# Kernel optimization log

Hardware: AMD Instinct MI355X
Metric: run time of the kernel (lower is better)

## Reference

```python
import jax, jax.numpy as jnp
import numpy as np

N_NODES = 50000
N_EDGES = 1_600_000
DIMS = [512, 2048, 1024, 512]  # input, hiddens..., output
NEG_SLOPE = 0.2
EPS = 1e-12


def setup_inputs() -> dict:
    key = jax.random.key(0)
    ks = jax.random.split(key, 12)
    inp = {
        "x": jax.random.normal(ks[0], (N_NODES, DIMS[0]), dtype=jnp.float32),
        "edge_row": jax.random.randint(ks[1], (N_EDGES,), 0, N_NODES, dtype=jnp.int32),
        "edge_col": jax.random.randint(ks[2], (N_EDGES,), 0, N_NODES, dtype=jnp.int32),
        "edge_val": jax.random.uniform(ks[3], (N_EDGES,), dtype=jnp.float32),
    }
    # GraphConvolution params per layer: W [d_in, d_out], b [d_out]
    for i in range(len(DIMS) - 1):
        d_in, d_out = DIMS[i], DIMS[i + 1]
        scale = 1.0 / np.sqrt(d_in)
        inp[f"W{i}"] = jax.random.uniform(ks[4 + 2 * i], (d_in, d_out), minval=-scale, maxval=scale, dtype=jnp.float32)
        inp[f"b{i}"] = jnp.zeros((d_out,), dtype=jnp.float32)
    return inp


def _spmm(edge_row, edge_col, edge_val, h):
    # out[i] = sum_{e: row[e]==i} val[e] * h[col[e]]   (sparse adj @ h)
    msgs = edge_val[:, None] * h[edge_col]  # [E, d]
    return jax.ops.segment_sum(msgs, edge_row, num_segments=N_NODES)


def reference(x, edge_row, edge_col, edge_val, W0, b0, W1, b1, W2, b2):
    Ws = [W0, W1, W2]
    bs = [b0, b1, b2]
    # F.normalize: L2-normalize each row
    norm = jnp.sqrt(jnp.sum(x * x, axis=1, keepdims=True))
    h = x / jnp.maximum(norm, EPS)
    n_layers = len(Ws)
    for i in range(n_layers):
        support = h @ Ws[i]                                  # [N, d_out]
        h = _spmm(edge_row, edge_col, edge_val, support) + bs[i]
        if i != n_layers - 1:
            # dropout is identity at inference; leaky_relu(0.2)
            h = jnp.where(h >= 0, h, NEG_SLOPE * h)
    return h
```

## Files before the change

### kernel.cpp

```cpp
#include <hip/hip_runtime.h>
#include <stdint.h>

#define N_NODES 50000
#define N_EDGES 1600000

typedef __attribute__((ext_vector_type(8))) short bf16x8;
typedef __attribute__((ext_vector_type(4))) float f32x4;
typedef __attribute__((ext_vector_type(8))) unsigned short u16x8;

__device__ __forceinline__ float b2f(unsigned short u) {
  union { unsigned int i; float f; } v; v.i = ((unsigned int)u) << 16; return v.f;
}
__device__ __forceinline__ unsigned short f2b(float f) {
  union { float f; unsigned int i; } v; v.f = f;
  unsigned int u = v.i;
  u += 0x7fffu + ((u >> 16) & 1u);
  return (unsigned short)(u >> 16);
}

__device__ __forceinline__ void load_lds16(const void* g, void* l) {
  __builtin_amdgcn_global_load_lds(
      (const __attribute__((address_space(1))) unsigned int*)g,
      (__attribute__((address_space(3))) unsigned int*)l, 16, 0, 0);
}

__global__ __launch_bounds__(256) void normalize_k(const float* __restrict__ x,
                                                   unsigned short* __restrict__ out) {
  int lane = threadIdx.x & 63;
  int row = blockIdx.x * 4 + (threadIdx.x >> 6);
  const float* p = x + (size_t)row * 512 + lane * 8;
  float4 a = ((const float4*)p)[0];
  float4 b = ((const float4*)p)[1];
  float ss = a.x*a.x + a.y*a.y + a.z*a.z + a.w*a.w
           + b.x*b.x + b.y*b.y + b.z*b.z + b.w*b.w;
#pragma unroll
  for (int off = 1; off < 64; off <<= 1) ss += __shfl_xor(ss, off, 64);
  float s = 1.0f / fmaxf(sqrtf(ss), 1e-12f);
  u16x8 o;
  o[0]=f2b(a.x*s); o[1]=f2b(a.y*s); o[2]=f2b(a.z*s); o[3]=f2b(a.w*s);
  o[4]=f2b(b.x*s); o[5]=f2b(b.y*s); o[6]=f2b(b.z*s); o[7]=f2b(b.w*s);
  *(u16x8*)(out + (size_t)row * 512 + lane * 8) = o;
}

__global__ __launch_bounds__(256) void hist_k(const int* __restrict__ er, int* __restrict__ deg) {
  int i = blockIdx.x * 256 + threadIdx.x;
  if (i < N_EDGES) atomicAdd(&deg[er[i]], 1);
}

__global__ __launch_bounds__(256) void scan1_k(const int* __restrict__ deg, int* __restrict__ out,
                                               int* __restrict__ csum, int n) {
  __shared__ int sd[256];
  int t = threadIdx.x;
  int base = blockIdx.x * 1024;
  int v[4], s = 0;
#pragma unroll
  for (int j = 0; j < 4; ++j) {
    int idx = base + t * 4 + j;
    v[j] = (idx < n) ? deg[idx] : 0;
    s += v[j];
  }
  sd[t] = s;
  __syncthreads();
  for (int off = 1; off < 256; off <<= 1) {
    int xx = (t >= off) ? sd[t - off] : 0;
    __syncthreads();
    sd[t] += xx;
    __syncthreads();
  }
  if (t == 255) csum[blockIdx.x] = sd[255];
  int run = sd[t] - s;
#pragma unroll
  for (int j = 0; j < 4; ++j) {
    int idx = base + t * 4 + j;
    if (idx < n) out[idx] = run;
    run += v[j];
  }
}

__global__ void scan2_k(int* csum, int n) {
  if (threadIdx.x == 0 && blockIdx.x == 0) {
    int s = 0;
    for (int i = 0; i < n; ++i) { int t = csum[i]; csum[i] = s; s += t; }
  }
}

__global__ __launch_bounds__(256) void scan3_k(int* __restrict__ out, const int* __restrict__ csum, int n) {
  int i = blockIdx.x * 256 + threadIdx.x;
  if (i < n) out[i] += csum[i >> 10];
}

__global__ __launch_bounds__(256) void scatter_k(const int* __restrict__ er, const int* __restrict__ ec,
    const float* __restrict__ ev, int* __restrict__ head,
    int* __restrict__ scol, float* __restrict__ sval) {
  int i = blockIdx.x * 256 + threadIdx.x;
  if (i < N_EDGES) {
    int r = er[i];
    int p = atomicAdd(&head[r], 1);
    scol[p] = ec[i];
    sval[p] = ev[i];
  }
}

__global__ __launch_bounds__(256) void wconv_k(const float* __restrict__ W,
                                               unsigned short* __restrict__ WT, int K, int N) {
  int i = blockIdx.x * 256 + threadIdx.x;
  if (i < N * K) {
    int n = i / K, k = i - n * K;
    WT[i] = f2b(W[(size_t)k * N + n]);
  }
}

template <int D, int MODE>
__global__ __launch_bounds__(256) void spmm_k(const unsigned short* __restrict__ in,
    const int* __restrict__ rs, const int* __restrict__ scol, const float* __restrict__ sval,
    const float* __restrict__ bias, void* __restrict__ outv) {
  constexpr int VE = D / 64;
  int lane = threadIdx.x & 63;
  int row = blockIdx.x * 4 + (threadIdx.x >> 6);
  int e0 = rs[row];
  int e1 = (row + 1 == N_NODES) ? N_EDGES : rs[row + 1];
  float acc[VE];
#pragma unroll
  for (int j = 0; j < VE; ++j) acc[j] = 0.f;
  const unsigned short* base = in + (size_t)lane * VE;
  for (int e = e0; e < e1; ++e) {
    int c = scol[e];
    float v = sval[e];
    const unsigned short* p = base + (size_t)c * D;
#pragma unroll
    for (int q = 0; q < VE / 8; ++q) {
      u16x8 u = *(const u16x8*)(p + q * 8);
#pragma unroll
      for (int h = 0; h < 8; ++h) acc[q * 8 + h] = fmaf(v, b2f(u[h]), acc[q * 8 + h]);
    }
  }
  size_t obase = (size_t)row * D + lane * VE;
  if (MODE == 2) {
    float* out = (float*)outv;
#pragma unroll
    for (int j = 0; j < VE; ++j) out[obase + j] = acc[j] + bias[lane * VE + j];
  } else {
    unsigned short* out = (unsigned short*)outv;
#pragma unroll
    for (int q = 0; q < VE / 8; ++q) {
      u16x8 o;
#pragma unroll
      for (int h = 0; h < 8; ++h) {
        float xo = acc[q * 8 + h];
        if (MODE == 1) {
          xo += bias[lane * VE + q * 8 + h];
          xo = xo >= 0.f ? xo : 0.2f * xo;
        }
        o[h] = f2b(xo);
      }
      *(u16x8*)(out + obase + q * 8) = o;
    }
  }
}

template <bool BIAS_RELU>
__global__ __launch_bounds__(256) void gemm_bt_k(
    const unsigned short* __restrict__ A, const unsigned short* __restrict__ BT,
    const float* __restrict__ bias, unsigned short* __restrict__ C,
    int M, int N, int K) {
  __shared__ __align__(16) unsigned short sA[128 * 32];
  __shared__ __align__(16) unsigned short sB[128 * 32];
  int tid = threadIdx.x;
  int lane = tid & 63;
  int wid = tid >> 6;
  int wm = (wid & 1) * 64;
  int wn = (wid >> 1) * 64;
  int mblk = blockIdx.y * 128;
  int nblk = blockIdx.x * 128;
  const unsigned short* Bb = BT + (size_t)nblk * K;
  int c0 = tid, c1 = tid + 256;
  int ar0 = c0 >> 2, ac0 = (c0 & 3) * 8;
  int ar1 = c1 >> 2, ac1 = (c1 & 3) * 8;
  int ra0 = mblk + ar0; if (ra0 > M - 1) ra0 = M - 1;
  int ra1 = mblk + ar1; if (ra1 > M - 1) ra1 = M - 1;
  f32x4 acc[4][4] = {};
  for (int k0 = 0; k0 < K; k0 += 32) {
    load_lds16(A + (size_t)ra0 * K + k0 + ac0, &sA[c0 * 8]);
    load_lds16(A + (size_t)ra1 * K + k0 + ac1, &sA[c1 * 8]);
    load_lds16(Bb + (size_t)ar0 * K + k0 + ac0, &sB[c0 * 8]);
    load_lds16(Bb + (size_t)ar1 * K + k0 + ac1, &sB[c1 * 8]);
    __syncthreads();
    bf16x8 af[4], bfr[4];
    int kq = (lane >> 4) * 8;
    int mr = wm + (lane & 15);
    int nr = wn + (lane & 15);
#pragma unroll
    for (int i = 0; i < 4; ++i) af[i] = *(const bf16x8*)&sA[(mr + i * 16) * 32 + kq];
#pragma unroll
    for (int j = 0; j < 4; ++j) bfr[j] = *(const bf16x8*)&sB[(nr + j * 16) * 32 + kq];
#pragma unroll
    for (int i = 0; i < 4; ++i)
#pragma unroll
      for (int j = 0; j < 4; ++j)
        acc[i][j] = __builtin_amdgcn_mfma_f32_16x16x32_bf16(af[i], bfr[j], acc[i][j], 0, 0, 0);
    __syncthreads();
  }
  int quad = lane >> 4;
  int lc = lane & 15;
#pragma unroll
  for (int i = 0; i < 4; ++i) {
#pragma unroll
    for (int r = 0; r < 4; ++r) {
      int gm = mblk + wm + i * 16 + quad * 4 + r;
      if (gm < M) {
#pragma unroll
        for (int j = 0; j < 4; ++j) {
          int gn = nblk + wn + j * 16 + lc;
          float v = acc[i][j][r];
          if (BIAS_RELU) { v += bias[gn]; v = v >= 0.f ? v : 0.2f * v; }
          C[(size_t)gm * N + gn] = f2b(v);
        }
      }
    }
  }
}

extern "C" void kernel_launch(void* const* d_in, const int* in_sizes, int n_in,
                              void* d_out, int out_size, void* d_ws, size_t ws_size,
                              hipStream_t stream) {
  (void)in_sizes; (void)n_in; (void)out_size; (void)ws_size;
  const float* x  = (const float*)d_in[0];
  const int* erow = (const int*)d_in[1];
  const int* ecol = (const int*)d_in[2];
  const float* ev = (const float*)d_in[3];
  const float* W0 = (const float*)d_in[4];
  const float* b0 = (const float*)d_in[5];
  const float* W1 = (const float*)d_in[6];
  const float* b1 = (const float*)d_in[7];
  const float* W2 = (const float*)d_in[8];
  const float* b2 = (const float*)d_in[9];

  char* ws = (char*)d_ws;
  unsigned short* norm_out  = (unsigned short*)(ws);
  unsigned short* spmm0_out = (unsigned short*)(ws + 51200000);
  unsigned short* h1chunk   = (unsigned short*)(ws + 102400000);
  unsigned short* h2        = (unsigned short*)(ws);
  unsigned short* vbuf      = (unsigned short*)(ws + 102400000);
  int*   scol = (int*)(ws + 153600000);
  float* sval = (float*)(ws + 160000000);
  int*   rs   = (int*)(ws + 166400000);
  int*   head = (int*)(ws + 166600192);
  int*   deg  = (int*)(ws + 166800384);
  int*   csum = (int*)(ws + 167000576);
  unsigned short* w0t = (unsigned short*)(ws + 167000832);
  unsigned short* w1t = w0t + (size_t)2048 * 512;
  unsigned short* w2t = w1t + (size_t)1024 * 2048;
  unsigned short* u   = (unsigned short*)d_out;

  hipMemsetAsync(deg, 0, N_NODES * 4, stream);
  hist_k<<<6250, 256, 0, stream>>>(erow, deg);
  scan1_k<<<49, 256, 0, stream>>>(deg, rs, csum, N_NODES);
  scan2_k<<<1, 64, 0, stream>>>(csum, 49);
  scan3_k<<<196, 256, 0, stream>>>(rs, csum, N_NODES);
  hipMemcpyAsync(head, rs, N_NODES * 4, hipMemcpyDeviceToDevice, stream);
  scatter_k<<<6250, 256, 0, stream>>>(erow, ecol, ev, head, scol, sval);

  wconv_k<<<4096, 256, 0, stream>>>(W0, w0t, 512, 2048);
  wconv_k<<<8192, 256, 0, stream>>>(W1, w1t, 2048, 1024);
  wconv_k<<<2048, 256, 0, stream>>>(W2, w2t, 1024, 512);

  normalize_k<<<12500, 256, 0, stream>>>(x, norm_out);

  spmm_k<512, 0><<<12500, 256, 0, stream>>>(norm_out, rs, scol, sval, nullptr, spmm0_out);

  for (int c = 0; c < 4; ++c) {
    const unsigned short* a0 = spmm0_out + (size_t)c * 12500 * 512;
    unsigned short* uc = u + (size_t)c * 12500 * 1024;
    gemm_bt_k<true ><<<dim3(16, 98), 256, 0, stream>>>(a0, w0t, b0, h1chunk, 12500, 2048, 512);
    gemm_bt_k<false><<<dim3(8, 98), 256, 0, stream>>>(h1chunk, w1t, nullptr, uc, 12500, 1024, 2048);
  }

  spmm_k<1024, 1><<<12500, 256, 0, stream>>>(u, rs, scol, sval, b1, h2);

  gemm_bt_k<false><<<dim3(4, 391), 256, 0, stream>>>(h2, w2t, nullptr, vbuf, N_NODES, 512, 1024);
  spmm_k<512, 2><<<12500, 256, 0, stream>>>(vbuf, rs, scol, sval, b2, (float*)d_out);
}
```

Measured before the change: 2.036 ms.

## Pack CSR edges as int2, unroll SpMM gathers by four, split wide rows into slices

Column index and edge value are now stored interleaved as an int2, so each edge needs one 8-byte load instead of two separate loads. The SpMM inner loop is unrolled by four so four row gathers are in flight at once, which should hide more gather latency. The 1024-wide SpMM is split into two 512-column slices over twice as many blocks, which keeps per-thread registers at 8 accumulators but reads each edge list twice.

```diff
diff --git a/kernel.cpp b/kernel.cpp
--- a/kernel.cpp
+++ b/kernel.cpp
@@ -90,14 +90,12 @@
 }
 
 __global__ __launch_bounds__(256) void scatter_k(const int* __restrict__ er, const int* __restrict__ ec,
-    const float* __restrict__ ev, int* __restrict__ head,
-    int* __restrict__ scol, float* __restrict__ sval) {
+    const float* __restrict__ ev, int* __restrict__ head, int2* __restrict__ ep) {
   int i = blockIdx.x * 256 + threadIdx.x;
   if (i < N_EDGES) {
     int r = er[i];
     int p = atomicAdd(&head[r], 1);
-    scol[p] = ec[i];
-    sval[p] = ev[i];
+    ep[p] = make_int2(ec[i], __float_as_int(ev[i]));
   }
 }
 
@@ -112,49 +110,65 @@
 
 template <int D, int MODE>
 __global__ __launch_bounds__(256) void spmm_k(const unsigned short* __restrict__ in,
-    const int* __restrict__ rs, const int* __restrict__ scol, const float* __restrict__ sval,
+    const int* __restrict__ rs, const int2* __restrict__ ep,
     const float* __restrict__ bias, void* __restrict__ outv) {
-  constexpr int VE = D / 64;
+  constexpr int NS = D / 512;
   int lane = threadIdx.x & 63;
-  int row = blockIdx.x * 4 + (threadIdx.x >> 6);
+  int blk = blockIdx.x;
+  int slice = (NS == 1) ? 0 : (blk / 12500);
+  int rowg = (NS == 1) ? blk : (blk - slice * 12500);
+  int row = rowg * 4 + (threadIdx.x >> 6);
   int e0 = rs[row];
   int e1 = (row + 1 == N_NODES) ? N_EDGES : rs[row + 1];
-  float acc[VE];
-#pragma unroll
-  for (int j = 0; j < VE; ++j) acc[j] = 0.f;
-  const unsigned short* base = in + (size_t)lane * VE;
-  for (int e = e0; e < e1; ++e) {
-    int c = scol[e];
-    float v = sval[e];
-    const unsigned short* p = base + (size_t)c * D;
-#pragma unroll
-    for (int q = 0; q < VE / 8; ++q) {
-      u16x8 u = *(const u16x8*)(p + q * 8);
-#pragma unroll
-      for (int h = 0; h < 8; ++h) acc[q * 8 + h] = fmaf(v, b2f(u[h]), acc[q * 8 + h]);
-    }
-  }
-  size_t obase = (size_t)row * D + lane * VE;
+  float acc[8] = {0.f, 0.f, 0.f, 0.f, 0.f, 0.f, 0.f, 0.f};
+  const unsigned short* base = in + (size_t)slice * 512 + (size_t)lane * 8;
+  int e = e0;
+  for (; e + 4 <= e1; e += 4) {
+    int2 p0 = ep[e];
+    int2 p1 = ep[e + 1];
+    int2 p2 = ep[e + 2];
+    int2 p3 = ep[e + 3];
+    u16x8 u0 = *(const u16x8*)(base + (size_t)p0.x * D);
+    u16x8 u1 = *(const u16x8*)(base + (size_t)p1.x * D);
+    u16x8 u2 = *(const u16x8*)(base + (size_t)p2.x * D);
+    u16x8 u3 = *(const u16x8*)(base + (size_t)p3.x * D);
+    float v0 = __int_as_float(p0.y), v1 = __int_as_float(p1.y);
+    float v2 = __int_as_float(p2.y), v3 = __int_as_float(p3.y);
+#pragma unroll
+    for (int h = 0; h < 8; ++h) acc[h] = fmaf(v0, b2f(u0[h]), acc[h]);
+#pragma unroll
+    for (int h = 0; h < 8; ++h) acc[h] = fmaf(v1, b2f(u1[h]), acc[h]);
+#pragma unroll
+    for (int h = 0; h < 8; ++h) acc[h] = fmaf(v2, b2f(u2[h]), acc[h]);
+#pragma unroll
+    for (int h = 0; h < 8; ++h) acc[h] = fmaf(v3, b2f(u3[h]), acc[h]);
+  }
+  for (; e < e1; ++e) {
+    int2 p = ep[e];
+    u16x8 u = *(const u16x8*)(base + (size_t)p.x * D);
+    float v = __int_as_float(p.y);
+#pragma unroll
+    for (int h = 0; h < 8; ++h) acc[h] = fmaf(v, b2f(u[h]), acc[h]);
+  }
+  size_t obase = (size_t)row * D + (size_t)slice * 512 + lane * 8;
+  int bbase = slice * 512 + lane * 8;
   if (MODE == 2) {
     float* out = (float*)outv;
 #pragma unroll
-    for (int j = 0; j < VE; ++j) out[obase + j] = acc[j] + bias[lane * VE + j];
+    for (int j = 0; j < 8; ++j) out[obase + j] = acc[j] + bias[bbase + j];
   } else {
     unsigned short* out = (unsigned short*)outv;
-#pragma unroll
-    for (int q = 0; q < VE / 8; ++q) {
-      u16x8 o;
-#pragma unroll
-      for (int h = 0; h < 8; ++h) {
-        float xo = acc[q * 8 + h];
-        if (MODE == 1) {
-          xo += bias[lane * VE + q * 8 + h];
-          xo = xo >= 0.f ? xo : 0.2f * xo;
-        }
-        o[h] = f2b(xo);
+    u16x8 o;
+#pragma unroll
+    for (int h = 0; h < 8; ++h) {
+      float xo = acc[h];
+      if (MODE == 1) {
+        xo += bias[bbase + h];
+        xo = xo >= 0.f ? xo : 0.2f * xo;
       }
-      *(u16x8*)(out + obase + q * 8) = o;
+      o[h] = f2b(xo);
     }
+    *(u16x8*)(out + obase) = o;
   }
 }
 
@@ -241,8 +255,7 @@
   unsigned short* h1chunk   = (unsigned short*)(ws + 102400000);
   unsigned short* h2        = (unsigned short*)(ws);
   unsigned short* vbuf      = (unsigned short*)(ws + 102400000);
-  int*   scol = (int*)(ws + 153600000);
-  float* sval = (float*)(ws + 160000000);
+  int2*  ep   = (int2*)(ws + 153600000);
   int*   rs   = (int*)(ws + 166400000);
   int*   head = (int*)(ws + 166600192);
   int*   deg  = (int*)(ws + 166800384);
@@ -258,7 +271,7 @@
   scan2_k<<<1, 64, 0, stream>>>(csum, 49);
   scan3_k<<<196, 256, 0, stream>>>(rs, csum, N_NODES);
   hipMemcpyAsync(head, rs, N_NODES * 4, hipMemcpyDeviceToDevice, stream);
-  scatter_k<<<6250, 256, 0, stream>>>(erow, ecol, ev, head, scol, sval);
+  scatter_k<<<6250, 256, 0, stream>>>(erow, ecol, ev, head, ep);
 
   wconv_k<<<4096, 256, 0, stream>>>(W0, w0t, 512, 2048);
   wconv_k<<<8192, 256, 0, stream>>>(W1, w1t, 2048, 1024);
@@ -266,7 +279,7 @@
 
   normalize_k<<<12500, 256, 0, stream>>>(x, norm_out);
 
-  spmm_k<512, 0><<<12500, 256, 0, stream>>>(norm_out, rs, scol, sval, nullptr, spmm0_out);
+  spmm_k<512, 0><<<12500, 256, 0, stream>>>(norm_out, rs, ep, nullptr, spmm0_out);
 
   for (int c = 0; c < 4; ++c) {
     const unsigned short* a0 = spmm0_out + (size_t)c * 12500 * 512;
@@ -275,8 +288,8 @@
     gemm_bt_k<false><<<dim3(8, 98), 256, 0, stream>>>(h1chunk, w1t, nullptr, uc, 12500, 1024, 2048);
   }
 
-  spmm_k<1024, 1><<<12500, 256, 0, stream>>>(u, rs, scol, sval, b1, h2);
+  spmm_k<1024, 1><<<25000, 256, 0, stream>>>(u, rs, ep, b1, h2);
 
   gemm_bt_k<false><<<dim3(4, 391), 256, 0, stream>>>(h2, w2t, nullptr, vbuf, N_NODES, 512, 1024);
-  spmm_k<512, 2><<<12500, 256, 0, stream>>>(vbuf, rs, scol, sval, b2, (float*)d_out);
-}
+  spmm_k<512, 2><<<12500, 256, 0, stream>>>(vbuf, rs, ep, b2, (float*)d_out);
+}
```

Result: no change. 2.034 ms (-0.1%).
